# Performance work log

Measured on AMD Instinct MI355X. Metric: run time of the kernel, lower is better.

## Reference

```python
import jax, jax.numpy as jnp
import numpy as np

B, H, S, DH = 8, 16, 512, 64
HID = H * DH


def setup_inputs() -> dict:
    key = jax.random.key(0)
    ks = jax.random.split(key, 16)
    # padding vectors: 1s up to a per-sample valid length, 0s afterwards
    # (first zero index == valid length, matching create_padding_matrix semantics)
    len_q = jax.random.randint(ks[0], (B,), S // 2, S + 1)
    len_k = jax.random.randint(ks[1], (B,), S // 2, S + 1)
    r = jnp.arange(S)
    pq = (r[None, :] < len_q[:, None]).astype(jnp.int32)
    pk = (r[None, :] < len_k[:, None]).astype(jnp.int32)
    sc = 0.02
    inp = {
        "padding_vector_q": pq,
        "padding_vector_k": pk,
        "query_t_1": jnp.zeros((1,), jnp.float32),
        "key_t": jnp.zeros((1,), jnp.float32),
        "hidden_states": jnp.zeros((1,), jnp.float32),
        "hidden_states_t_1": jnp.zeros((1,), jnp.float32),
        "hidden_from_last": jax.random.normal(ks[2], (B, H, S, DH), jnp.float32),
        "hidden_current": jax.random.normal(ks[3], (B, H, S, DH), jnp.float32),
        "max_n_codes": S,
        "interpretabity": 0,
        "iter_idx": 0,
        "W_v1": jax.random.normal(ks[4], (HID, HID), jnp.float32) * sc,
        "b_v1": jnp.zeros((HID,), jnp.float32),
        "W_v": jax.random.normal(ks[5], (HID, HID), jnp.float32) * sc,
        "b_v": jnp.zeros((HID,), jnp.float32),
        "W_q": jax.random.normal(ks[6], (HID, HID), jnp.float32) * sc,
        "b_q": jnp.zeros((HID,), jnp.float32),
        "W_k": jax.random.normal(ks[7], (HID, HID), jnp.float32) * sc,
        "b_k": jnp.zeros((HID,), jnp.float32),
        "W_cat": jax.random.normal(ks[8], (2 * DH, DH), jnp.float32) * sc,
        "b_cat": jnp.zeros((DH,), jnp.float32),
    }
    return inp


def reference(padding_vector_q, padding_vector_k, query_t_1, key_t,
              hidden_states, hidden_states_t_1, hidden_from_last, hidden_current,
              max_n_codes, interpretabity, iter_idx,
              W_v1, b_v1, W_v, b_v, W_q, b_q, W_k, b_k, W_cat, b_cat):
    b, h, s, dh = hidden_from_last.shape
    hid = h * dh
    # permute(0,2,1,3).flatten(start_dim=2): [B,H,S,Dh] -> [B,S,H*Dh]
    flat_last = hidden_from_last.transpose(0, 2, 1, 3).reshape(b, s, hid)
    flat_cur = hidden_current.transpose(0, 2, 1, 3).reshape(b, s, hid)

    def heads(x):  # [B,S,HID] -> [B,H,S,Dh]
        return x.reshape(b, s, h, dh).transpose(0, 2, 1, 3)

    v1 = heads(flat_last @ W_v1 + b_v1)   # value_t_1(hidden_from_last)
    vt = heads(flat_cur @ W_v + b_v)      # value(hidden_current)
    q = heads(flat_last @ W_q + b_q)
    k = heads(flat_cur @ W_k + b_k)

    scores = jnp.einsum('bhqd,bhkd->bhqk', q, k) / jnp.sqrt(jnp.float32(dh))
    scores_t = scores.transpose(0, 1, 3, 2)  # [B,H,Sk,Sq] (original permute(0,1,3,2))

    # vectorized per-sample padding mask: valid window [0:padd_q, 0:padd_k]
    def first_zero(v):
        hz = jnp.any(v == 0, axis=1)
        return jnp.where(hz, jnp.argmax(v == 0, axis=1), s)

    pq_len = first_zero(padding_vector_q)
    pk_len = first_zero(padding_vector_k)
    r = jnp.arange(s)
    valid = (r[None, :, None] < pq_len[:, None, None]) & \
            (r[None, None, :] < pk_len[:, None, None])  # [B,S,S]
    mask = (~valid)[:, None, :, :]  # True = masked, broadcast over heads

    # -1e9 underflows to exactly 0 after softmax in fp32, matching the
    # masked_fill(-inf) -> softmax -> masked_fill(0) chain without NaN rows
    NEG = jnp.float32(-1e9)
    attn = jax.nn.softmax(jnp.where(mask, NEG, scores_t), axis=-1)
    attention_values = jnp.where(mask, jnp.float32(0), attn)

    context_layer = jnp.einsum('bhks,bhsd->bhkd', attention_values, v1)
    context_layer2 = jnp.concatenate([context_layer, vt], axis=-1) @ W_cat + b_cat
    return attention_values, scores_t, context_layer2, context_layer
```

## Files before the change

### kernel.cpp

```cpp
#include <hip/hip_runtime.h>
#include <cstddef>

#define NB 8
#define NH 16
#define NS 512
#define NDH 64
#define NHID 1024
#define NBH (NB*NH)

#define QKV_ELEMS (NB*NH*NS*NDH)
#define ATTN_ELEMS ((size_t)NB*NH*(size_t)NS*NS)

typedef __bf16 bf16;
typedef __attribute__((ext_vector_type(8))) __bf16 bf16x8;
typedef __attribute__((ext_vector_type(4))) __bf16 bf16x4;
typedef __attribute__((ext_vector_type(4))) float f32x4;

__device__ __forceinline__ int swz(int idx, int row) { return idx ^ ((row & 7) << 3); }

__global__ void lens_kernel(const int* __restrict__ pq, const int* __restrict__ pk,
                            int* __restrict__ lens) {
    int bi = blockIdx.x;
    const int* v = (bi < NB) ? pq : pk;
    int b = bi & (NB - 1);
    int lane = threadIdx.x;
    int local = NS;
#pragma unroll
    for (int p = 0; p < NS / 64; ++p) {
        int idx = p * 64 + lane;
        if (v[b * NS + idx] == 0 && idx < local) local = idx;
    }
#pragma unroll
    for (int m = 32; m >= 1; m >>= 1) {
        int o = __shfl_xor(local, m, 64);
        local = min(local, o);
    }
    if (lane == 0) lens[bi] = local;
}

__global__ __launch_bounds__(256) void proj_kernel(
    const float* __restrict__ hl, const float* __restrict__ hc,
    const float* __restrict__ Wq, const float* __restrict__ bq,
    const float* __restrict__ Wk, const float* __restrict__ bk,
    const float* __restrict__ Wv1, const float* __restrict__ bv1,
    const float* __restrict__ Wv, const float* __restrict__ bv,
    bf16* __restrict__ oq, bf16* __restrict__ ok,
    bf16* __restrict__ ov1, bf16* __restrict__ ovt) {
    __shared__ bf16 As[128 * 32];
    __shared__ bf16 Bs[128 * 32];
    const float* src; const float* W; const float* bias; bf16* dst;
    switch (blockIdx.z) {
        case 0: src = hl; W = Wq;  bias = bq;  dst = oq;  break;
        case 1: src = hc; W = Wk;  bias = bk;  dst = ok;  break;
        case 2: src = hl; W = Wv1; bias = bv1; dst = ov1; break;
        default: src = hc; W = Wv;  bias = bv;  dst = ovt; break;
    }
    int t = threadIdx.x;
    int lane = t & 63, w = t >> 6;
    int wm = w & 1, wn = w >> 1;
    int m0 = blockIdx.y * 128, n0 = blockIdx.x * 128;
    f32x4 acc[4][4];
#pragma unroll
    for (int i = 0; i < 4; ++i)
#pragma unroll
        for (int j = 0; j < 4; ++j) acc[i][j] = (f32x4){0.f, 0.f, 0.f, 0.f};

    for (int k0 = 0; k0 < NHID; k0 += 32) {
#pragma unroll
        for (int p = 0; p < 4; ++p) {
            int f = p * 256 + t;
            int row = f >> 3, c4 = (f & 7) * 4;
            int m = m0 + row, b = m >> 9, s = m & (NS - 1);
            int c = k0 + c4;
            float4 v = *(const float4*)&src[(((size_t)b * NH + (c >> 6)) * NS + s) * NDH + (c & 63)];
            bf16x4 h;
            h[0] = (bf16)v.x; h[1] = (bf16)v.y; h[2] = (bf16)v.z; h[3] = (bf16)v.w;
            *(bf16x4*)&As[swz(row * 32 + c4, row)] = h;
        }
#pragma unroll
        for (int p = 0; p < 4; ++p) {
            int f = p * 256 + t;
            int n = f & 127, kk = (f >> 7) * 4;
            const float* wp = &W[(size_t)(k0 + kk) * NHID + n0 + n];
            bf16x4 h;
            h[0] = (bf16)wp[0]; h[1] = (bf16)wp[NHID];
            h[2] = (bf16)wp[2 * NHID]; h[3] = (bf16)wp[3 * NHID];
            *(bf16x4*)&Bs[swz(n * 32 + kk, n)] = h;
        }
        __syncthreads();
        int kb8 = (lane >> 4) * 8;
        bf16x8 a[4], bfr[4];
#pragma unroll
        for (int i = 0; i < 4; ++i) {
            int row = wm * 64 + i * 16 + (lane & 15);
            a[i] = *(const bf16x8*)&As[swz(row * 32 + kb8, row)];
        }
#pragma unroll
        for (int j = 0; j < 4; ++j) {
            int nr = wn * 64 + j * 16 + (lane & 15);
            bfr[j] = *(const bf16x8*)&Bs[swz(nr * 32 + kb8, nr)];
        }
#pragma unroll
        for (int i = 0; i < 4; ++i)
#pragma unroll
            for (int j = 0; j < 4; ++j)
                acc[i][j] = __builtin_amdgcn_mfma_f32_16x16x32_bf16(a[i], bfr[j], acc[i][j], 0, 0, 0);
        __syncthreads();
    }
    float bs[4];
#pragma unroll
    for (int j = 0; j < 4; ++j) bs[j] = bias[n0 + wn * 64 + j * 16 + (lane & 15)];
#pragma unroll
    for (int i = 0; i < 4; ++i)
#pragma unroll
        for (int r = 0; r < 4; ++r) {
            int m = m0 + wm * 64 + i * 16 + (lane >> 4) * 4 + r;
            int b = m >> 9, s = m & (NS - 1);
#pragma unroll
            for (int j = 0; j < 4; ++j) {
                int n = n0 + wn * 64 + j * 16 + (lane & 15);
                dst[(((size_t)b * NH + (n >> 6)) * NS + s) * NDH + (n & 63)] =
                    (bf16)(acc[i][j][r] + bs[j]);
            }
        }
}

__global__ __launch_bounds__(256) void attn_kernel(
    const bf16* __restrict__ qb, const bf16* __restrict__ kb,
    const int* __restrict__ lens,
    float* __restrict__ scores, float* __restrict__ attn) {
    __shared__ bf16 Ks[64 * 64];
    __shared__ float redm[4][64];
    __shared__ float reds[4][64];
    int bh = blockIdx.y, ki0 = blockIdx.x * 64;
    int b = bh >> 4;
    int t = threadIdx.x, lane = t & 63, w = t >> 6;
    int lq = lens[b], lk = lens[NB + b];
    const bf16* kbb = kb + ((size_t)bh * NS + ki0) * NDH;
    const bf16* qbb = qb + (size_t)bh * NS * NDH;
#pragma unroll
    for (int p = 0; p < 2; ++p) {
        int f = p * 256 + t;
        int row = f >> 3, d8 = (f & 7) * 8;
        bf16x8 v = *(const bf16x8*)&kbb[(size_t)row * NDH + d8];
        *(bf16x8*)&Ks[swz(row * 64 + d8, row)] = v;
    }
    __syncthreads();
    f32x4 acc[4][8];
#pragma unroll
    for (int i = 0; i < 4; ++i)
#pragma unroll
        for (int j = 0; j < 8; ++j) acc[i][j] = (f32x4){0.f, 0.f, 0.f, 0.f};
#pragma unroll
    for (int ds = 0; ds < 2; ++ds) {
        int kofs = ds * 32 + (lane >> 4) * 8;
        bf16x8 a[4];
#pragma unroll
        for (int i = 0; i < 4; ++i) {
            int row = i * 16 + (lane & 15);
            a[i] = *(const bf16x8*)&Ks[swz(row * 64 + kofs, row)];
        }
#pragma unroll
        for (int j = 0; j < 8; ++j) {
            int qi = w * 128 + j * 16 + (lane & 15);
            bf16x8 bq8 = *(const bf16x8*)&qbb[(size_t)qi * NDH + kofs];
#pragma unroll
            for (int i = 0; i < 4; ++i)
                acc[i][j] = __builtin_amdgcn_mfma_f32_16x16x32_bf16(a[i], bq8, acc[i][j], 0, 0, 0);
        }
    }
    int g = lane >> 4, c = lane & 15;
    float pmax[4][4];
#pragma unroll
    for (int i = 0; i < 4; ++i)
#pragma unroll
        for (int r = 0; r < 4; ++r) pmax[i][r] = -3.0e38f;
#pragma unroll
    for (int i = 0; i < 4; ++i)
#pragma unroll
        for (int j = 0; j < 8; ++j) {
            int qi = w * 128 + j * 16 + c;
            bool colv = qi < lk;
#pragma unroll
            for (int r = 0; r < 4; ++r) {
                float s = acc[i][j][r] * 0.125f;
                acc[i][j][r] = s;
                scores[((size_t)bh * NS + ki0 + i * 16 + g * 4 + r) * NS + qi] = s;
                if (colv) pmax[i][r] = fmaxf(pmax[i][r], s);
            }
        }
#pragma unroll
    for (int msk = 8; msk >= 1; msk >>= 1)
#pragma unroll
        for (int i = 0; i < 4; ++i)
#pragma unroll
            for (int r = 0; r < 4; ++r)
                pmax[i][r] = fmaxf(pmax[i][r], __shfl_xor(pmax[i][r], msk, 64));
    if (c == 0)
#pragma unroll
        for (int i = 0; i < 4; ++i)
#pragma unroll
            for (int r = 0; r < 4; ++r) redm[w][i * 16 + g * 4 + r] = pmax[i][r];
    __syncthreads();
    float rmax[4][4];
#pragma unroll
    for (int i = 0; i < 4; ++i)
#pragma unroll
        for (int r = 0; r < 4; ++r) {
            int row = i * 16 + g * 4 + r;
            rmax[i][r] = fmaxf(fmaxf(redm[0][row], redm[1][row]),
                               fmaxf(redm[2][row], redm[3][row]));
        }
    float psum[4][4];
#pragma unroll
    for (int i = 0; i < 4; ++i)
#pragma unroll
        for (int r = 0; r < 4; ++r) psum[i][r] = 0.f;
#pragma unroll
    for (int i = 0; i < 4; ++i)
#pragma unroll
        for (int j = 0; j < 8; ++j) {
            int qi = w * 128 + j * 16 + c;
            bool colv = qi < lk;
#pragma unroll
            for (int r = 0; r < 4; ++r) {
                float e = colv ? __expf(acc[i][j][r] - rmax[i][r]) : 0.f;
                acc[i][j][r] = e;
                psum[i][r] += e;
            }
        }
#pragma unroll
    for (int msk = 8; msk >= 1; msk >>= 1)
#pragma unroll
        for (int i = 0; i < 4; ++i)
#pragma unroll
            for (int r = 0; r < 4; ++r)
                psum[i][r] += __shfl_xor(psum[i][r], msk, 64);
    if (c == 0)
#pragma unroll
        for (int i = 0; i < 4; ++i)
#pragma unroll
            for (int r = 0; r < 4; ++r) reds[w][i * 16 + g * 4 + r] = psum[i][r];
    __syncthreads();
#pragma unroll
    for (int i = 0; i < 4; ++i)
#pragma unroll
        for (int r = 0; r < 4; ++r) {
            int row = i * 16 + g * 4 + r;
            float rs = reds[0][row] + reds[1][row] + reds[2][row] + reds[3][row];
            float inv = (rs > 0.f) ? 1.f / rs : 0.f;
            bool rowv = (ki0 + row) < lq;
#pragma unroll
            for (int j = 0; j < 8; ++j) {
                int qi = w * 128 + j * 16 + c;
                float v = rowv ? acc[i][j][r] * inv : 0.f;
                attn[((size_t)bh * NS + ki0 + row) * NS + qi] = v;
            }
        }
}

__global__ __launch_bounds__(256) void context_kernel(
    const float* __restrict__ attn, const bf16* __restrict__ v1,
    float* __restrict__ ctx) {
    __shared__ bf16 Ash[64 * 64];
    __shared__ bf16 Vs[64 * 64];
    int bh = blockIdx.y, ki0 = blockIdx.x * 64;
    int t = threadIdx.x, lane = t & 63, w = t >> 6;
    const float* ab = attn + ((size_t)bh * NS + ki0) * NS;
    const bf16* vb = v1 + (size_t)bh * NS * NDH;
    f32x4 acc[4];
#pragma unroll
    for (int j = 0; j < 4; ++j) acc[j] = (f32x4){0.f, 0.f, 0.f, 0.f};

    for (int q0 = 0; q0 < NS; q0 += 64) {
#pragma unroll
        for (int p = 0; p < 4; ++p) {
            int f = p * 256 + t;
            int row = f >> 4, c4 = (f & 15) * 4;
            float4 v = *(const float4*)&ab[(size_t)row * NS + q0 + c4];
            bf16x4 h;
            h[0] = (bf16)v.x; h[1] = (bf16)v.y; h[2] = (bf16)v.z; h[3] = (bf16)v.w;
            *(bf16x4*)&Ash[swz(row * 64 + c4, row)] = h;
        }
#pragma unroll
        for (int p = 0; p < 2; ++p) {
            int f = p * 256 + t;
            int qr = f >> 3, d8 = (f & 7) * 8;
            bf16x8 v = *(const bf16x8*)&vb[(size_t)(q0 + qr) * NDH + d8];
#pragma unroll
            for (int e = 0; e < 8; ++e) {
                int d = d8 + e;
                Vs[swz(d * 64 + qr, d)] = v[e];
            }
        }
        __syncthreads();
#pragma unroll
        for (int kk = 0; kk < 2; ++kk) {
            int kofs = kk * 32 + (lane >> 4) * 8;
            int arow = w * 16 + (lane & 15);
            bf16x8 a = *(const bf16x8*)&Ash[swz(arow * 64 + kofs, arow)];
#pragma unroll
            for (int j = 0; j < 4; ++j) {
                int d = j * 16 + (lane & 15);
                bf16x8 bv8 = *(const bf16x8*)&Vs[swz(d * 64 + kofs, d)];
                acc[j] = __builtin_amdgcn_mfma_f32_16x16x32_bf16(a, bv8, acc[j], 0, 0, 0);
            }
        }
        __syncthreads();
    }
    int g = lane >> 4, c = lane & 15;
#pragma unroll
    for (int j = 0; j < 4; ++j)
#pragma unroll
        for (int r = 0; r < 4; ++r) {
            int ki = ki0 + w * 16 + g * 4 + r;
            ctx[((size_t)bh * NS + ki) * NDH + j * 16 + c] = acc[j][r];
        }
}

__global__ __launch_bounds__(256) void cat_kernel(
    const float* __restrict__ ctx, const bf16* __restrict__ vt,
    const float* __restrict__ Wcat, const float* __restrict__ bcat,
    float* __restrict__ out) {
    __shared__ float As[16][68];
    __shared__ float Bs[16][68];
    int t = threadIdx.x;
    int tx = t & 15, ty = t >> 4;
    int row0 = blockIdx.x * 64;
    float acc[4][4];
#pragma unroll
    for (int i = 0; i < 4; ++i)
#pragma unroll
        for (int j = 0; j < 4; ++j) acc[i][j] = 0.f;

    for (int k0 = 0; k0 < 2 * NDH; k0 += 16) {
#pragma unroll
        for (int p = 0; p < 4; ++p) {
            int e = p * 256 + t;
            int kk = e & 15, mm = e >> 4;
            int cidx = k0 + kk;
            float val = (cidx < NDH) ? ctx[(size_t)(row0 + mm) * NDH + cidx]
                                     : (float)vt[(size_t)(row0 + mm) * NDH + (cidx - NDH)];
            As[kk][mm] = val;
        }
#pragma unroll
        for (int p = 0; p < 4; ++p) {
            int e = p * 256 + t;
            int nn = e & 63, kk = e >> 6;
            Bs[kk][nn] = Wcat[(size_t)(k0 + kk) * NDH + nn];
        }
        __syncthreads();
#pragma unroll
        for (int kk = 0; kk < 16; ++kk) {
            float a[4], bb[4];
            *(float4*)&a[0]  = *(const float4*)&As[kk][ty * 4];
            *(float4*)&bb[0] = *(const float4*)&Bs[kk][tx * 4];
#pragma unroll
            for (int i = 0; i < 4; ++i)
#pragma unroll
                for (int j = 0; j < 4; ++j) acc[i][j] += a[i] * bb[j];
        }
        __syncthreads();
    }
#pragma unroll
    for (int i = 0; i < 4; ++i) {
        int n = tx * 4;
        float4 o;
        o.x = acc[i][0] + bcat[n + 0];
        o.y = acc[i][1] + bcat[n + 1];
        o.z = acc[i][2] + bcat[n + 2];
        o.w = acc[i][3] + bcat[n + 3];
        *(float4*)&out[(size_t)(row0 + ty * 4 + i) * NDH + n] = o;
    }
}

extern "C" void kernel_launch(void* const* d_in, const int* in_sizes, int n_in,
                              void* d_out, int out_size, void* d_ws, size_t ws_size,
                              hipStream_t stream) {
    (void)in_sizes; (void)n_in; (void)out_size; (void)ws_size;
    const int*   pq   = (const int*)d_in[0];
    const int*   pk   = (const int*)d_in[1];
    const float* hl   = (const float*)d_in[6];
    const float* hc   = (const float*)d_in[7];
    const float* Wv1  = (const float*)d_in[11];
    const float* bv1  = (const float*)d_in[12];
    const float* Wv   = (const float*)d_in[13];
    const float* bv   = (const float*)d_in[14];
    const float* Wq   = (const float*)d_in[15];
    const float* bq   = (const float*)d_in[16];
    const float* Wk   = (const float*)d_in[17];
    const float* bk   = (const float*)d_in[18];
    const float* Wcat = (const float*)d_in[19];
    const float* bcat = (const float*)d_in[20];

    float* out_attn   = (float*)d_out;
    float* out_scores = out_attn + ATTN_ELEMS;
    float* out_ctx2   = out_attn + 2 * ATTN_ELEMS;
    float* out_ctx    = out_ctx2 + QKV_ELEMS;

    bf16*  qb     = (bf16*)d_ws;
    bf16*  kbp    = qb + QKV_ELEMS;
    float* ctx_ws = (float*)d_ws;
    int*   lens   = (int*)((char*)d_ws + (size_t)QKV_ELEMS * sizeof(float));
    bf16*  v1b    = (bf16*)out_ctx;
    bf16*  vtb    = v1b + QKV_ELEMS;

    lens_kernel<<<16, 64, 0, stream>>>(pq, pk, lens);
    proj_kernel<<<dim3(8, 32, 4), 256, 0, stream>>>(
        hl, hc, Wq, bq, Wk, bk, Wv1, bv1, Wv, bv, qb, kbp, v1b, vtb);
    attn_kernel<<<dim3(8, NBH), 256, 0, stream>>>(qb, kbp, lens, out_scores, out_attn);
    context_kernel<<<dim3(8, NBH), 256, 0, stream>>>(out_attn, v1b, ctx_ws);
    cat_kernel<<<(NB * NH * NS) / 64, 256, 0, stream>>>(ctx_ws, vtb, Wcat, bcat, out_ctx2);
    hipMemcpyAsync(out_ctx, ctx_ws, (size_t)QKV_ELEMS * sizeof(float),
                   hipMemcpyDeviceToDevice, stream);
}
```

Before: 546.3 us.

## Pre-convert projection operands to bf16 and stream tiles into LDS directly

New measurement: 512.5 us. 1.07x faster.

```diff
diff --git a/kernel.cpp b/kernel.cpp
--- a/kernel.cpp
+++ b/kernel.cpp
@@ -15,6 +15,13 @@
 typedef __attribute__((ext_vector_type(8))) __bf16 bf16x8;
 typedef __attribute__((ext_vector_type(4))) __bf16 bf16x4;
 typedef __attribute__((ext_vector_type(4))) float f32x4;
+typedef unsigned int u32;
+
+__device__ __forceinline__ void gload_lds16(const void* g, void* l) {
+    __builtin_amdgcn_global_load_lds(
+        (const __attribute__((address_space(1))) u32*)g,
+        (__attribute__((address_space(3))) u32*)l, 16, 0, 0);
+}
 
 __device__ __forceinline__ int swz(int idx, int row) { return idx ^ ((row & 7) << 3); }
 
@@ -38,78 +45,114 @@
     if (lane == 0) lens[bi] = local;
 }
 
+__global__ __launch_bounds__(256) void cvtA_kernel(
+    const float* __restrict__ hl, const float* __restrict__ hc,
+    bf16* __restrict__ al, bf16* __restrict__ ac) {
+    const float* src = blockIdx.z ? hc : hl;
+    bf16* dst = blockIdx.z ? ac : al;
+    int tid = blockIdx.x * 256 + threadIdx.x;
+    int d8 = tid & 7, s = (tid >> 3) & 511, h = (tid >> 12) & 15, b = tid >> 16;
+    const float* p = &src[(((size_t)b * NH + h) * NS + s) * NDH + d8 * 8];
+    float4 v0 = *(const float4*)p;
+    float4 v1 = *(const float4*)(p + 4);
+    bf16x8 o;
+    o[0] = (bf16)v0.x; o[1] = (bf16)v0.y; o[2] = (bf16)v0.z; o[3] = (bf16)v0.w;
+    o[4] = (bf16)v1.x; o[5] = (bf16)v1.y; o[6] = (bf16)v1.z; o[7] = (bf16)v1.w;
+    *(bf16x8*)&dst[((size_t)(b * NS + s)) * NHID + h * NDH + d8 * 8] = o;
+}
+
+__global__ __launch_bounds__(256) void cvtW_kernel(
+    const float* __restrict__ Wq, const float* __restrict__ Wk,
+    const float* __restrict__ Wv1, const float* __restrict__ Wv,
+    bf16* __restrict__ Wt) {
+    const float* W;
+    switch (blockIdx.z) {
+        case 0: W = Wq; break;
+        case 1: W = Wk; break;
+        case 2: W = Wv1; break;
+        default: W = Wv; break;
+    }
+    bf16* out = Wt + (size_t)blockIdx.z * NHID * NHID;
+    __shared__ bf16 T[64][72];
+    int t = threadIdx.x;
+    int k0 = blockIdx.y * 64, n0 = blockIdx.x * 64;
+#pragma unroll
+    for (int p = 0; p < 4; ++p) {
+        int kk = p * 16 + (t >> 4), c4 = (t & 15) * 4;
+        float4 v = *(const float4*)&W[(size_t)(k0 + kk) * NHID + n0 + c4];
+        T[c4 + 0][kk] = (bf16)v.x;
+        T[c4 + 1][kk] = (bf16)v.y;
+        T[c4 + 2][kk] = (bf16)v.z;
+        T[c4 + 3][kk] = (bf16)v.w;
+    }
+    __syncthreads();
+#pragma unroll
+    for (int p = 0; p < 2; ++p) {
+        int f = p * 256 + t;
+        int nn = f >> 3, k8 = (f & 7) * 8;
+        bf16x8 o;
+#pragma unroll
+        for (int e = 0; e < 8; ++e) o[e] = T[nn][k8 + e];
+        *(bf16x8*)&out[(size_t)(n0 + nn) * NHID + k0 + k8] = o;
+    }
+}
+
 __global__ __launch_bounds__(256) void proj_kernel(
-    const float* __restrict__ hl, const float* __restrict__ hc,
-    const float* __restrict__ Wq, const float* __restrict__ bq,
-    const float* __restrict__ Wk, const float* __restrict__ bk,
-    const float* __restrict__ Wv1, const float* __restrict__ bv1,
-    const float* __restrict__ Wv, const float* __restrict__ bv,
+    const bf16* __restrict__ al, const bf16* __restrict__ ac,
+    const bf16* __restrict__ Wt,
+    const float* __restrict__ bq, const float* __restrict__ bk,
+    const float* __restrict__ bv1, const float* __restrict__ bv,
     bf16* __restrict__ oq, bf16* __restrict__ ok,
     bf16* __restrict__ ov1, bf16* __restrict__ ovt) {
-    __shared__ bf16 As[128 * 32];
-    __shared__ bf16 Bs[128 * 32];
-    const float* src; const float* W; const float* bias; bf16* dst;
+    __shared__ bf16 As[128 * 64];
+    __shared__ bf16 Bs[128 * 64];
+    const bf16* A; const bf16* W; const float* bias; bf16* dst;
     switch (blockIdx.z) {
-        case 0: src = hl; W = Wq;  bias = bq;  dst = oq;  break;
-        case 1: src = hc; W = Wk;  bias = bk;  dst = ok;  break;
-        case 2: src = hl; W = Wv1; bias = bv1; dst = ov1; break;
-        default: src = hc; W = Wv;  bias = bv;  dst = ovt; break;
-    }
-    int t = threadIdx.x;
-    int lane = t & 63, w = t >> 6;
+        case 0: A = al; W = Wt;                 bias = bq;  dst = oq;  break;
+        case 1: A = ac; W = Wt + 1048576;       bias = bk;  dst = ok;  break;
+        case 2: A = al; W = Wt + 2097152;       bias = bv1; dst = ov1; break;
+        default: A = ac; W = Wt + 3145728;      bias = bv;  dst = ovt; break;
+    }
+    int t = threadIdx.x, lane = t & 63, w = t >> 6;
     int wm = w & 1, wn = w >> 1;
     int m0 = blockIdx.y * 128, n0 = blockIdx.x * 128;
+    int lrow = lane >> 3, lk8 = (lane & 7) * 8;
     f32x4 acc[4][4];
 #pragma unroll
     for (int i = 0; i < 4; ++i)
 #pragma unroll
         for (int j = 0; j < 4; ++j) acc[i][j] = (f32x4){0.f, 0.f, 0.f, 0.f};
 
-    for (int k0 = 0; k0 < NHID; k0 += 32) {
-#pragma unroll
-        for (int p = 0; p < 4; ++p) {
-            int f = p * 256 + t;
-            int row = f >> 3, c4 = (f & 7) * 4;
-            int m = m0 + row, b = m >> 9, s = m & (NS - 1);
-            int c = k0 + c4;
-            float4 v = *(const float4*)&src[(((size_t)b * NH + (c >> 6)) * NS + s) * NDH + (c & 63)];
-            bf16x4 h;
-            h[0] = (bf16)v.x; h[1] = (bf16)v.y; h[2] = (bf16)v.z; h[3] = (bf16)v.w;
-            *(bf16x4*)&As[swz(row * 32 + c4, row)] = h;
-        }
-#pragma unroll
-        for (int p = 0; p < 4; ++p) {
-            int f = p * 256 + t;
-            int n = f & 127, kk = (f >> 7) * 4;
-            const float* wp = &W[(size_t)(k0 + kk) * NHID + n0 + n];
-            bf16x4 h;
-            h[0] = (bf16)wp[0]; h[1] = (bf16)wp[NHID];
-            h[2] = (bf16)wp[2 * NHID]; h[3] = (bf16)wp[3 * NHID];
-            *(bf16x4*)&Bs[swz(n * 32 + kk, n)] = h;
-        }
-        __syncthreads();
-        int kb8 = (lane >> 4) * 8;
-        bf16x8 a[4], bfr[4];
+    for (int kb = 0; kb < NHID; kb += 64) {
 #pragma unroll
         for (int i = 0; i < 4; ++i) {
-            int row = wm * 64 + i * 16 + (lane & 15);
-            a[i] = *(const bf16x8*)&As[swz(row * 32 + kb8, row)];
-        }
-#pragma unroll
-        for (int j = 0; j < 4; ++j) {
-            int nr = wn * 64 + j * 16 + (lane & 15);
-            bfr[j] = *(const bf16x8*)&Bs[swz(nr * 32 + kb8, nr)];
-        }
-#pragma unroll
-        for (int i = 0; i < 4; ++i)
+            int seg = w * 2048 + i * 512;
+            int row = (w * 32 + i * 8) + lrow;
+            gload_lds16(&A[(size_t)(m0 + row) * NHID + kb + lk8], &As[seg]);
+            gload_lds16(&W[(size_t)(n0 + row) * NHID + kb + lk8], &Bs[seg]);
+        }
+        __syncthreads();
+#pragma unroll
+        for (int ks = 0; ks < 2; ++ks) {
+            int ko = ks * 32 + (lane >> 4) * 8;
+            bf16x8 a[4], bb[4];
+#pragma unroll
+            for (int i = 0; i < 4; ++i)
+                a[i] = *(const bf16x8*)&As[(wm * 64 + i * 16 + (lane & 15)) * 64 + ko];
 #pragma unroll
             for (int j = 0; j < 4; ++j)
-                acc[i][j] = __builtin_amdgcn_mfma_f32_16x16x32_bf16(a[i], bfr[j], acc[i][j], 0, 0, 0);
-        __syncthreads();
-    }
-    float bs[4];
-#pragma unroll
-    for (int j = 0; j < 4; ++j) bs[j] = bias[n0 + wn * 64 + j * 16 + (lane & 15)];
+                bb[j] = *(const bf16x8*)&Bs[(wn * 64 + j * 16 + (lane & 15)) * 64 + ko];
+#pragma unroll
+            for (int i = 0; i < 4; ++i)
+#pragma unroll
+                for (int j = 0; j < 4; ++j)
+                    acc[i][j] = __builtin_amdgcn_mfma_f32_16x16x32_bf16(a[i], bb[j], acc[i][j], 0, 0, 0);
+        }
+        __syncthreads();
+    }
+    float bsv[4];
+#pragma unroll
+    for (int j = 0; j < 4; ++j) bsv[j] = bias[n0 + wn * 64 + j * 16 + (lane & 15)];
 #pragma unroll
     for (int i = 0; i < 4; ++i)
 #pragma unroll
@@ -120,7 +163,7 @@
             for (int j = 0; j < 4; ++j) {
                 int n = n0 + wn * 64 + j * 16 + (lane & 15);
                 dst[(((size_t)b * NH + (n >> 6)) * NS + s) * NDH + (n & 63)] =
-                    (bf16)(acc[i][j][r] + bs[j]);
+                    (bf16)(acc[i][j][r] + bsv[j]);
             }
         }
 }
@@ -398,19 +441,22 @@
     float* out_ctx2   = out_attn + 2 * ATTN_ELEMS;
     float* out_ctx    = out_ctx2 + QKV_ELEMS;
 
-    bf16*  qb     = (bf16*)d_ws;
-    bf16*  kbp    = qb + QKV_ELEMS;
-    float* ctx_ws = (float*)d_ws;
-    int*   lens   = (int*)((char*)d_ws + (size_t)QKV_ELEMS * sizeof(float));
-    bf16*  v1b    = (bf16*)out_ctx;
-    bf16*  vtb    = v1b + QKV_ELEMS;
+    char* ws = (char*)d_ws;
+    bf16* al   = (bf16*)(ws);
+    bf16* acb  = (bf16*)(ws + 8388608);
+    bf16* WtB  = (bf16*)(ws + 16777216);
+    bf16* qb   = (bf16*)(ws + 25165824);
+    bf16* kbp  = (bf16*)(ws + 33554432);
+    bf16* v1b  = (bf16*)(ws + 41943040);
+    bf16* vtb  = (bf16*)(ws + 50331648);
+    int*  lens = (int*)(ws + 58720256);
 
     lens_kernel<<<16, 64, 0, stream>>>(pq, pk, lens);
+    cvtA_kernel<<<dim3(2048, 1, 2), 256, 0, stream>>>(hl, hc, al, acb);
+    cvtW_kernel<<<dim3(16, 16, 4), 256, 0, stream>>>(Wq, Wk, Wv1, Wv, WtB);
     proj_kernel<<<dim3(8, 32, 4), 256, 0, stream>>>(
-        hl, hc, Wq, bq, Wk, bk, Wv1, bv1, Wv, bv, qb, kbp, v1b, vtb);
+        al, acb, WtB, bq, bk, bv1, bv, qb, kbp, v1b, vtb);
     attn_kernel<<<dim3(8, NBH), 256, 0, stream>>>(qb, kbp, lens, out_scores, out_attn);
-    context_kernel<<<dim3(8, NBH), 256, 0, stream>>>(out_attn, v1b, ctx_ws);
-    cat_kernel<<<(NB * NH * NS) / 64, 256, 0, stream>>>(ctx_ws, vtb, Wcat, bcat, out_ctx2);
-    hipMemcpyAsync(out_ctx, ctx_ws, (size_t)QKV_ELEMS * sizeof(float),
-                   hipMemcpyDeviceToDevice, stream);
-}
+    context_kernel<<<dim3(8, NBH), 256, 0, stream>>>(out_attn, v1b, out_ctx);
+    cat_kernel<<<(NB * NH * NS) / 64, 256, 0, stream>>>(out_ctx, vtb, Wcat, bcat, out_ctx2);
+}
```
